# Kernel optimization log

Measured on AMD Instinct MI355X. Metric: run time of the kernel, lower is better.

## Reference

```python
import jax, jax.numpy as jnp
import numpy as np

N = 16384   # must equal C**2 so the rel-pos embed broadcasts with x
C = 128     # in_channels
K = 9       # k (min legal for C=128: (2k-1)^2 >= 2C-1)
C_OUT = 256


def setup_inputs() -> dict:
    key = jax.random.key(0)
    k1, k2, k3 = jax.random.split(key, 3)
    x = jax.random.normal(k1, (N, C), dtype=jnp.float32)
    rel_pos_table = jax.random.normal(k2, ((2 * K - 1) ** 2, C), dtype=jnp.float32) * 0.02
    W = jax.random.normal(k3, (2 * C, C_OUT), dtype=jnp.float32) / np.float32(np.sqrt(2 * C))
    b = jnp.zeros((C_OUT,), dtype=jnp.float32)
    return {"x": x, "rel_pos_table": rel_pos_table, "W": W, "b": b}


def _knn_indices(x, k):
    # brute-force kNN (torch_cluster knn_graph, loop=False), dilation=1 -> no edge subsampling
    sq = jnp.sum(x * x, axis=-1)                       # [N]
    d = sq[:, None] + sq[None, :] - 2.0 * (x @ x.T)    # [N, N] squared distances
    d = d.at[jnp.diag_indices(x.shape[0])].set(jnp.inf)  # exclude self-loops
    _, idx = jax.lax.top_k(-d, k)                      # [N, k] nearest neighbors
    return idx


def reference(x, rel_pos_table, W, b):
    n, c = x.shape
    # 1) graph built on RAW x (before rel-pos add), as in the torch forward
    nbr = _knn_indices(x, K)                           # [N, K]
    # 2) learnable relative positional embedding: grid_size = x.shape[1] = C
    ar = jnp.arange(c)
    rel = (ar[:, None] - ar[None, :] + c - 1).reshape(-1)  # [C*C] == [N]
    x = x + rel_pos_table[rel]                         # [N, C]
    # 3) MRConv: max-relative aggregation + concat + 1x1 linear
    x_j = x[nbr]                                       # [N, K, C] neighbor gather
    m = jnp.max(x_j - x[:, None, :], axis=1)           # [N, C] max over neighbors
    return jnp.concatenate([x, m], axis=-1) @ W + b    # [N, C_OUT]
```

## Files before the change

kernel.cpp:

```cpp
#include <hip/hip_runtime.h>

#define NPTS 16384
#define CH 128
#define KNN 9
#define NCAND 12
#define NHALF 4
#define COUT 256
#define RG 16
#define RCAND 3

typedef __attribute__((ext_vector_type(8))) short bf16x8;
typedef __attribute__((ext_vector_type(4))) float f32x4;
typedef __attribute__((address_space(1))) const unsigned gu32;
typedef __attribute__((address_space(3))) unsigned lu32;


__device__ __forceinline__ unsigned bfhi2(float x0, float x1) {
    unsigned u0 = __float_as_uint(x0), u1 = __float_as_uint(x1);
    unsigned r0 = (u0 + 0x7fffu + ((u0 >> 16) & 1u));
    unsigned r1 = (u1 + 0x7fffu + ((u1 >> 16) & 1u));
    return (r0 >> 16) | (r1 & 0xffff0000u);
}

struct TopL {
    float l0,l1,l2,l3,l4,l5,l6,l7,l8,l9,la,lb;
    int   m0,m1,m2,m3,m4,m5,m6,m7,m8,m9,ma,mb;
};
struct Top9 {
    float l0,l1,l2,l3,l4,l5,l6,l7,l8;
    int   m0,m1,m2,m3,m4,m5,m6,m7,m8;
};

__device__ __forceinline__ bool lexlt(float d, int g, float L, int M) {
    return d < L || (d == L && g < M);
}

__device__ __forceinline__ void ins12(TopL& T, float d, int g) {
    if (!lexlt(d, g, T.lb, T.mb)) return;
    bool b0 = lexlt(d,g,T.l0,T.m0);
    bool b1 = lexlt(d,g,T.l1,T.m1);
    bool b2 = lexlt(d,g,T.l2,T.m2);
    bool b3 = lexlt(d,g,T.l3,T.m3);
    bool b4 = lexlt(d,g,T.l4,T.m4);
    bool b5 = lexlt(d,g,T.l5,T.m5);
    bool b6 = lexlt(d,g,T.l6,T.m6);
    bool b7 = lexlt(d,g,T.l7,T.m7);
    bool b8 = lexlt(d,g,T.l8,T.m8);
    bool b9 = lexlt(d,g,T.l9,T.m9);
    bool ba = lexlt(d,g,T.la,T.ma);
    T.lb = ba ? T.la : d;               T.mb = ba ? T.ma : g;
    T.la = b9 ? T.l9 : (ba ? d : T.la); T.ma = b9 ? T.m9 : (ba ? g : T.ma);
    T.l9 = b8 ? T.l8 : (b9 ? d : T.l9); T.m9 = b8 ? T.m8 : (b9 ? g : T.m9);
    T.l8 = b7 ? T.l7 : (b8 ? d : T.l8); T.m8 = b7 ? T.m7 : (b8 ? g : T.m8);
    T.l7 = b6 ? T.l6 : (b7 ? d : T.l7); T.m7 = b6 ? T.m6 : (b7 ? g : T.m7);
    T.l6 = b5 ? T.l5 : (b6 ? d : T.l6); T.m6 = b5 ? T.m5 : (b6 ? g : T.m6);
    T.l5 = b4 ? T.l4 : (b5 ? d : T.l5); T.m5 = b4 ? T.m4 : (b5 ? g : T.m5);
    T.l4 = b3 ? T.l3 : (b4 ? d : T.l4); T.m4 = b3 ? T.m3 : (b4 ? g : T.m4);
    T.l3 = b2 ? T.l2 : (b3 ? d : T.l3); T.m3 = b2 ? T.m2 : (b3 ? g : T.m3);
    T.l2 = b1 ? T.l1 : (b2 ? d : T.l2); T.m2 = b1 ? T.m1 : (b2 ? g : T.m2);
    T.l1 = b0 ? T.l0 : (b1 ? d : T.l1); T.m1 = b0 ? T.m0 : (b1 ? g : T.m1);
    T.l0 = b0 ? d : T.l0;               T.m0 = b0 ? g : T.m0;
}

__device__ __forceinline__ void ins9(Top9& T, float d, int g) {
    if (!lexlt(d, g, T.l8, T.m8)) return;
    bool b0 = lexlt(d,g,T.l0,T.m0);
    bool b1 = lexlt(d,g,T.l1,T.m1);
    bool b2 = lexlt(d,g,T.l2,T.m2);
    bool b3 = lexlt(d,g,T.l3,T.m3);
    bool b4 = lexlt(d,g,T.l4,T.m4);
    bool b5 = lexlt(d,g,T.l5,T.m5);
    bool b6 = lexlt(d,g,T.l6,T.m6);
    bool b7 = lexlt(d,g,T.l7,T.m7);
    T.l8 = b7 ? T.l7 : d;               T.m8 = b7 ? T.m7 : g;
    T.l7 = b6 ? T.l6 : (b7 ? d : T.l7); T.m7 = b6 ? T.m6 : (b7 ? g : T.m7);
    T.l6 = b5 ? T.l5 : (b6 ? d : T.l6); T.m6 = b5 ? T.m5 : (b6 ? g : T.m6);
    T.l5 = b4 ? T.l4 : (b5 ? d : T.l5); T.m5 = b4 ? T.m4 : (b5 ? g : T.m5);
    T.l4 = b3 ? T.l3 : (b4 ? d : T.l4); T.m4 = b3 ? T.m3 : (b4 ? g : T.m4);
    T.l3 = b2 ? T.l2 : (b3 ? d : T.l3); T.m3 = b2 ? T.m2 : (b3 ? g : T.m3);
    T.l2 = b1 ? T.l1 : (b2 ? d : T.l2); T.m2 = b1 ? T.m1 : (b2 ? g : T.m2);
    T.l1 = b0 ? T.l0 : (b1 ? d : T.l1); T.m1 = b0 ? T.m0 : (b1 ? g : T.m1);
    T.l0 = b0 ? d : T.l0;               T.m0 = b0 ? g : T.m0;
}

__device__ __forceinline__ void merge_shfl(TopL& T, int mask) {
    TopL o;
    o.l0=__shfl_xor(T.l0,mask); o.m0=__shfl_xor(T.m0,mask);
    o.l1=__shfl_xor(T.l1,mask); o.m1=__shfl_xor(T.m1,mask);
    o.l2=__shfl_xor(T.l2,mask); o.m2=__shfl_xor(T.m2,mask);
    o.l3=__shfl_xor(T.l3,mask); o.m3=__shfl_xor(T.m3,mask);
    o.l4=__shfl_xor(T.l4,mask); o.m4=__shfl_xor(T.m4,mask);
    o.l5=__shfl_xor(T.l5,mask); o.m5=__shfl_xor(T.m5,mask);
    o.l6=__shfl_xor(T.l6,mask); o.m6=__shfl_xor(T.m6,mask);
    o.l7=__shfl_xor(T.l7,mask); o.m7=__shfl_xor(T.m7,mask);
    o.l8=__shfl_xor(T.l8,mask); o.m8=__shfl_xor(T.m8,mask);
    o.l9=__shfl_xor(T.l9,mask); o.m9=__shfl_xor(T.m9,mask);
    o.la=__shfl_xor(T.la,mask); o.ma=__shfl_xor(T.ma,mask);
    o.lb=__shfl_xor(T.lb,mask); o.mb=__shfl_xor(T.mb,mask);
    ins12(T,o.l0,o.m0); ins12(T,o.l1,o.m1); ins12(T,o.l2,o.m2);
    ins12(T,o.l3,o.m3); ins12(T,o.l4,o.m4); ins12(T,o.l5,o.m5);
    ins12(T,o.l6,o.m6); ins12(T,o.l7,o.m7); ins12(T,o.l8,o.m8);
    ins12(T,o.l9,o.m9); ins12(T,o.la,o.ma); ins12(T,o.lb,o.mb);
}

__device__ __forceinline__ void merge_shfl9(Top9& T, int mask) {
    Top9 o;
    o.l0=__shfl_xor(T.l0,mask); o.m0=__shfl_xor(T.m0,mask);
    o.l1=__shfl_xor(T.l1,mask); o.m1=__shfl_xor(T.m1,mask);
    o.l2=__shfl_xor(T.l2,mask); o.m2=__shfl_xor(T.m2,mask);
    o.l3=__shfl_xor(T.l3,mask); o.m3=__shfl_xor(T.m3,mask);
    o.l4=__shfl_xor(T.l4,mask); o.m4=__shfl_xor(T.m4,mask);
    o.l5=__shfl_xor(T.l5,mask); o.m5=__shfl_xor(T.m5,mask);
    o.l6=__shfl_xor(T.l6,mask); o.m6=__shfl_xor(T.m6,mask);
    o.l7=__shfl_xor(T.l7,mask); o.m7=__shfl_xor(T.m7,mask);
    o.l8=__shfl_xor(T.l8,mask); o.m8=__shfl_xor(T.m8,mask);
    ins9(T,o.l0,o.m0); ins9(T,o.l1,o.m1); ins9(T,o.l2,o.m2);
    ins9(T,o.l3,o.m3); ins9(T,o.l4,o.m4); ins9(T,o.l5,o.m5);
    ins9(T,o.l6,o.m6); ins9(T,o.l7,o.m7); ins9(T,o.l8,o.m8);
}

__global__ __launch_bounds__(256) void sqnp_kernel(const float* __restrict__ x,
                                                   float* __restrict__ sq) {
    const int i = blockIdx.x * 256 + threadIdx.x;
    const float4* row4 = (const float4*)(x + (size_t)i * CH);
    float r[8];
    {
        float4 a = row4[0], b = row4[1];
        r[0] = __fmul_rn(a.x, a.x); r[1] = __fmul_rn(a.y, a.y);
        r[2] = __fmul_rn(a.z, a.z); r[3] = __fmul_rn(a.w, a.w);
        r[4] = __fmul_rn(b.x, b.x); r[5] = __fmul_rn(b.y, b.y);
        r[6] = __fmul_rn(b.z, b.z); r[7] = __fmul_rn(b.w, b.w);
    }
#pragma unroll
    for (int g = 1; g < 16; ++g) {
        float4 a = row4[2 * g], b = row4[2 * g + 1];
        r[0] = __fadd_rn(r[0], __fmul_rn(a.x, a.x));
        r[1] = __fadd_rn(r[1], __fmul_rn(a.y, a.y));
        r[2] = __fadd_rn(r[2], __fmul_rn(a.z, a.z));
        r[3] = __fadd_rn(r[3], __fmul_rn(a.w, a.w));
        r[4] = __fadd_rn(r[4], __fmul_rn(b.x, b.x));
        r[5] = __fadd_rn(r[5], __fmul_rn(b.y, b.y));
        r[6] = __fadd_rn(r[6], __fmul_rn(b.z, b.z));
        r[7] = __fadd_rn(r[7], __fmul_rn(b.w, b.w));
    }
    float t0 = __fadd_rn(__fadd_rn(r[0], r[1]), __fadd_rn(r[2], r[3]));
    float t1 = __fadd_rn(__fadd_rn(r[4], r[5]), __fadd_rn(r[6], r[7]));
    sq[i] = __fadd_rn(t0, t1);
}

__global__ __launch_bounds__(256) void split_kernel(const float* __restrict__ x,
                                                    short* __restrict__ xhi) {
    const int P = blockIdx.x * 256 + threadIdx.x;
    const int r = P >> 4;
    const int s = P & 15;
    const int phys = s ^ (r & 15);
    const float4* src = (const float4*)(x + (size_t)r * CH) + s * 2;
    float4 f0 = src[0], f1 = src[1];
    uint4 h;
    h.x = bfhi2(f0.x, f0.y);
    h.y = bfhi2(f0.z, f0.w);
    h.z = bfhi2(f1.x, f1.y);
    h.w = bfhi2(f1.z, f1.w);
    *(uint4*)&xhi[(size_t)r * 128 + phys * 8] = h;
}

__global__ __launch_bounds__(256, 3) void knn_kernel(const short* __restrict__ xhi,
                                                     const float* __restrict__ sq,
                                                     unsigned short* __restrict__ cand) {
    __shared__ short Bhi[64 * 128];
    __shared__ float Dist[64 * 64];
    const int t = threadIdx.x;
    const int row0 = blockIdx.x * 64;
    const int half = blockIdx.y;
    const int ctbeg = half * (NPTS / NHALF);
    const int ctend = ctbeg + NPTS / NHALF;

    const int lane = t & 63;
    const int w = t >> 6;
    const int m = lane & 15;
    const int quad = lane >> 4;

#pragma unroll
    for (int it = 0; it < 4; ++it) {
        const int P = t + it * 256;
        __builtin_amdgcn_global_load_lds(
            (gu32*)&xhi[(size_t)ctbeg * 128 + P * 8],
            (lu32*)&Bhi[(it * 256 + w * 64) * 8], 16, 0, 0);
    }
    const short* arow = xhi + (size_t)(row0 + 16 * w + m) * 128;
    const bf16x8 a0 = *(const bf16x8*)&arow[((0 * 4 + quad) ^ m) * 8];
    const bf16x8 a1 = *(const bf16x8*)&arow[((1 * 4 + quad) ^ m) * 8];
    const bf16x8 a2 = *(const bf16x8*)&arow[((2 * 4 + quad) ^ m) * 8];
    const bf16x8 a3 = *(const bf16x8*)&arow[((3 * 4 + quad) ^ m) * 8];

    TopL T;
    T.l0=T.l1=T.l2=T.l3=T.l4=T.l5=T.l6=T.l7=T.l8=T.l9=T.la=T.lb = __builtin_inff();
    T.m0=T.m1=T.m2=T.m3=T.m4=T.m5=T.m6=T.m7=T.m8=T.m9=T.ma=T.mb = 0x7fffffff;

    const int srow = t >> 2;
    const int sq4 = t & 3;
    const int srowg = row0 + srow;
    const float* drow = &Dist[srow * 64];
    const int sxor = srow & 63;

    float qd0 = __builtin_inff(), qd1 = __builtin_inff();
    int   qg0 = 0x7fffffff,      qg1 = 0x7fffffff;
    int   qn = 0;

    for (int ct = ctbeg; ct < ctend; ct += 64) {
        __syncthreads();

        const float sqc0 = sq[ct + 0  + m];
        const float sqc1 = sq[ct + 16 + m];
        const float sqc2 = sq[ct + 32 + m];
        const float sqc3 = sq[ct + 48 + m];

        f32x4 acc0 = {0.f,0.f,0.f,0.f};
        f32x4 acc1 = {0.f,0.f,0.f,0.f};
        f32x4 acc2 = {0.f,0.f,0.f,0.f};
        f32x4 acc3 = {0.f,0.f,0.f,0.f};

#pragma unroll
        for (int kc = 0; kc < 4; ++kc) {
            const int ks = ((kc * 4 + quad) ^ m) * 8;
            const bf16x8 ah = (kc == 0) ? a0 : (kc == 1) ? a1 : (kc == 2) ? a2 : a3;
            bf16x8 bh0 = *(const bf16x8*)&Bhi[(0  + m) * 128 + ks];
            bf16x8 bh1 = *(const bf16x8*)&Bhi[(16 + m) * 128 + ks];
            bf16x8 bh2 = *(const bf16x8*)&Bhi[(32 + m) * 128 + ks];
            bf16x8 bh3 = *(const bf16x8*)&Bhi[(48 + m) * 128 + ks];
            acc0 = __builtin_amdgcn_mfma_f32_16x16x32_bf16(ah, bh0, acc0, 0, 0, 0);
            acc1 = __builtin_amdgcn_mfma_f32_16x16x32_bf16(ah, bh1, acc1, 0, 0, 0);
            acc2 = __builtin_amdgcn_mfma_f32_16x16x32_bf16(ah, bh2, acc2, 0, 0, 0);
            acc3 = __builtin_amdgcn_mfma_f32_16x16x32_bf16(ah, bh3, acc3, 0, 0, 0);
        }

#pragma unroll
        for (int reg = 0; reg < 4; ++reg) {
            const int row = 16 * w + quad * 4 + reg;
            const int c0 = 0  + m;
            const int c1 = 16 + m;
            const int c2 = 32 + m;
            const int c3 = 48 + m;
            Dist[row * 64 + (c0 ^ row)] = __builtin_fmaf(-2.f, acc0[reg], sqc0);
            Dist[row * 64 + (c1 ^ row)] = __builtin_fmaf(-2.f, acc1[reg], sqc1);
            Dist[row * 64 + (c2 ^ row)] = __builtin_fmaf(-2.f, acc2[reg], sqc2);
            Dist[row * 64 + (c3 ^ row)] = __builtin_fmaf(-2.f, acc3[reg], sqc3);
        }
        __syncthreads();

        const int ctn = ct + 64;
        if (ctn < ctend) {
#pragma unroll
            for (int it = 0; it < 4; ++it) {
                const int P = t + it * 256;
                __builtin_amdgcn_global_load_lds(
                    (gu32*)&xhi[(size_t)ctn * 128 + P * 8],
                    (lu32*)&Bhi[(it * 256 + w * 64) * 8], 16, 0, 0);
            }
        }

#pragma unroll
        for (int k = 0; k < 16; ++k) {
            const int col = sq4 * 16 + k;
            const float d = drow[col ^ sxor];
            const int cg = ct + col;
            const bool pass = (d <= T.lb) && (cg != srowg);
            if (pass) {
                if (qn >= 2) {
                    ins12(T, d, cg);
                } else if (qn == 0) {
                    qd0 = d; qg0 = cg;
                } else {
                    qd1 = d; qg1 = cg;
                }
                ++qn;
            }
        }
        if (__any(qn >= 2)) {
            ins12(T, qd0, qg0);
            ins12(T, qd1, qg1);
            qd0 = qd1 = __builtin_inff();
            qg0 = qg1 = 0x7fffffff;
            qn = 0;
        }
    }

    ins12(T, qd0, qg0);
    ins12(T, qd1, qg1);
    merge_shfl(T, 1);
    merge_shfl(T, 2);

    if (sq4 == 0) {
        unsigned short* cp_out = cand + (size_t)srowg * (NHALF * NCAND) + half * NCAND;
        cp_out[0]=(unsigned short)T.m0; cp_out[1]=(unsigned short)T.m1;
        cp_out[2]=(unsigned short)T.m2; cp_out[3]=(unsigned short)T.m3;
        cp_out[4]=(unsigned short)T.m4; cp_out[5]=(unsigned short)T.m5;
        cp_out[6]=(unsigned short)T.m6; cp_out[7]=(unsigned short)T.m7;
        cp_out[8]=(unsigned short)T.m8; cp_out[9]=(unsigned short)T.m9;
        cp_out[10]=(unsigned short)T.ma; cp_out[11]=(unsigned short)T.mb;
    }
}

__global__ __launch_bounds__(256) void refine_np_kernel(const float* __restrict__ x,
                                                        const float* __restrict__ sq,
                                                        const unsigned short* __restrict__ cand,
                                                        unsigned short* __restrict__ nbr) {
    const int gt = blockIdx.x * 256 + threadIdx.x;
    const int i = gt >> 4;
    const int g = gt & (RG - 1);
    const float4* X4 = (const float4*)x;
    const float sqi = sq[i];

    int ci[RCAND];
#pragma unroll
    for (int m = 0; m < RCAND; ++m)
        ci[m] = (int)cand[i * (NHALF * NCAND) + g * RCAND + m];
    float dot[RCAND];
#pragma unroll
    for (int m = 0; m < RCAND; ++m) dot[m] = 0.f;
#pragma unroll 4
    for (int c4 = 0; c4 < 32; ++c4) {
        float4 xv = X4[(size_t)i * 32 + c4];
#pragma unroll
        for (int m = 0; m < RCAND; ++m) {
            float4 nv = X4[(size_t)ci[m] * 32 + c4];
            float a = dot[m];
            a = __builtin_fmaf(xv.x, nv.x, a);
            a = __builtin_fmaf(xv.y, nv.y, a);
            a = __builtin_fmaf(xv.z, nv.z, a);
            a = __builtin_fmaf(xv.w, nv.w, a);
            dot[m] = a;
        }
    }

    Top9 T;
    T.l0=T.l1=T.l2=T.l3=T.l4=T.l5=T.l6=T.l7=T.l8 = __builtin_inff();
    T.m0=T.m1=T.m2=T.m3=T.m4=T.m5=T.m6=T.m7=T.m8 = 0x7fffffff;
#pragma unroll
    for (int m = 0; m < RCAND; ++m) {
        float s = __fadd_rn(sqi, sq[ci[m]]);
        float d = __fsub_rn(s, __fmul_rn(2.0f, dot[m]));
        ins9(T, d, ci[m]);
    }

    merge_shfl9(T, 1);
    merge_shfl9(T, 2);
    merge_shfl9(T, 4);
    merge_shfl9(T, 8);

    if (g == 0) {
        unsigned short* np = nbr + (size_t)i * KNN;
        np[0]=(unsigned short)T.m0; np[1]=(unsigned short)T.m1; np[2]=(unsigned short)T.m2;
        np[3]=(unsigned short)T.m3; np[4]=(unsigned short)T.m4; np[5]=(unsigned short)T.m5;
        np[6]=(unsigned short)T.m6; np[7]=(unsigned short)T.m7; np[8]=(unsigned short)T.m8;
    }
}

__global__ __launch_bounds__(256, 2) void out_kernel(const float* __restrict__ x,
                                                     const float* __restrict__ tab,
                                                     const float* __restrict__ W,
                                                     const float* __restrict__ bias,
                                                     const unsigned short* __restrict__ nbr,
                                                     float* __restrict__ out) {
    __shared__ float cat[32][260];
    const int t = threadIdx.x;
    const int row0 = blockIdx.x * 32;
    {
        const int row = t >> 3;
        const int q = t & 7;
        const int i = row0 + row;
        const int rel_i = (i >> 7) - (i & 127) + 127;
        int nb[KNN], reln[KNN];
#pragma unroll
        for (int j = 0; j < KNN; ++j) {
            nb[j] = (int)nbr[i * KNN + j];
            reln[j] = (nb[j] >> 7) - (nb[j] & 127) + 127;
        }
        const float4* X4 = (const float4*)x;
        const float4* T4 = (const float4*)tab;
#pragma unroll
        for (int cc = 0; cc < 4; ++cc) {
            const int c4 = q * 4 + cc;
            float4 xv = X4[i * 32 + c4];
            float4 tv = T4[rel_i * 32 + c4];
            float4 xi;
            xi.x = xv.x + tv.x; xi.y = xv.y + tv.y; xi.z = xv.z + tv.z; xi.w = xv.w + tv.w;
            const float ninf = -__builtin_inff();
            float4 mx = {ninf, ninf, ninf, ninf};
#pragma unroll
            for (int j = 0; j < KNN; ++j) {
                float4 nv = X4[nb[j] * 32 + c4];
                float4 ntv = T4[reln[j] * 32 + c4];
                mx.x = fmaxf(mx.x, nv.x + ntv.x - xi.x);
                mx.y = fmaxf(mx.y, nv.y + ntv.y - xi.y);
                mx.z = fmaxf(mx.z, nv.z + ntv.z - xi.z);
                mx.w = fmaxf(mx.w, nv.w + ntv.w - xi.w);
            }
            *(float4*)&cat[row][c4 * 4] = xi;
            *(float4*)&cat[row][CH + c4 * 4] = mx;
        }
    }
    __syncthreads();

    float acc[32];
    const float bo = bias[t];
#pragma unroll
    for (int i = 0; i < 32; ++i) acc[i] = bo;
#pragma unroll 2
    for (int c0 = 0; c0 < 2 * CH; c0 += 4) {
        const float w0 = W[(c0 + 0) * COUT + t];
        const float w1 = W[(c0 + 1) * COUT + t];
        const float w2 = W[(c0 + 2) * COUT + t];
        const float w3 = W[(c0 + 3) * COUT + t];
#pragma unroll
        for (int i = 0; i < 32; ++i) {
            const float4 cv = *(const float4*)&cat[i][c0];
            acc[i] = fmaf(cv.x, w0, acc[i]);
            acc[i] = fmaf(cv.y, w1, acc[i]);
            acc[i] = fmaf(cv.z, w2, acc[i]);
            acc[i] = fmaf(cv.w, w3, acc[i]);
        }
    }
#pragma unroll
    for (int i = 0; i < 32; ++i) out[(size_t)(row0 + i) * COUT + t] = acc[i];
}

extern "C" void kernel_launch(void* const* d_in, const int* in_sizes, int n_in,
                              void* d_out, int out_size, void* d_ws, size_t ws_size,
                              hipStream_t stream) {
    (void)in_sizes; (void)n_in; (void)out_size; (void)ws_size;
    const float* x = (const float*)d_in[0];
    const float* tab = (const float*)d_in[1];
    const float* W = (const float*)d_in[2];
    const float* b = (const float*)d_in[3];
    float* out = (float*)d_out;

    char* ws = (char*)d_ws;
    float* sq = (float*)ws;
    unsigned short* nbr = (unsigned short*)(sq + NPTS);

    short* xhi = (short*)d_out;
    unsigned short* cand = (unsigned short*)((char*)d_out + ((size_t)NPTS * CH * 2));

    sqnp_kernel<<<NPTS / 256, 256, 0, stream>>>(x, sq);
    split_kernel<<<NPTS * 16 / 256, 256, 0, stream>>>(x, xhi);
    knn_kernel<<<dim3(NPTS / 64, NHALF), 256, 0, stream>>>(xhi, sq, cand);
    refine_np_kernel<<<NPTS * RG / 256, 256, 0, stream>>>(x, sq, cand, nbr);
    out_kernel<<<NPTS / 32, 256, 0, stream>>>(x, tab, W, b, nbr, out);
}
```

Baseline: 632.7 us.

## Select kNN candidates directly from MFMA registers and split candidate range eightfold

The kNN kernel no longer stages the distance tile through a shared-memory Dist buffer. The MFMA operands are swapped so each lane holds distances for its own query row, and each lane filters candidates straight from the accumulator registers, with top-12 lists merged across quads by shuffles. The candidate range is also split into 8 slices instead of 4, with refine candidates scaled to match, to add grid parallelism. This removes LDS writes, reads and bank traffic and frees LDS for occupancy, at the cost of more candidates to refine and larger per-row candidate output.

```diff
diff --git a/kernel.cpp b/kernel.cpp
--- a/kernel.cpp
+++ b/kernel.cpp
@@ -4,10 +4,10 @@
 #define CH 128
 #define KNN 9
 #define NCAND 12
-#define NHALF 4
+#define NHALF 8
 #define COUT 256
 #define RG 16
-#define RCAND 3
+#define RCAND 6
 
 typedef __attribute__((ext_vector_type(8))) short bf16x8;
 typedef __attribute__((ext_vector_type(4))) float f32x4;
@@ -168,7 +168,6 @@
                                                      const float* __restrict__ sq,
                                                      unsigned short* __restrict__ cand) {
     __shared__ short Bhi[64 * 128];
-    __shared__ float Dist[64 * 64];
     const int t = threadIdx.x;
     const int row0 = blockIdx.x * 64;
     const int half = blockIdx.y;
@@ -187,21 +186,17 @@
             (gu32*)&xhi[(size_t)ctbeg * 128 + P * 8],
             (lu32*)&Bhi[(it * 256 + w * 64) * 8], 16, 0, 0);
     }
-    const short* arow = xhi + (size_t)(row0 + 16 * w + m) * 128;
-    const bf16x8 a0 = *(const bf16x8*)&arow[((0 * 4 + quad) ^ m) * 8];
-    const bf16x8 a1 = *(const bf16x8*)&arow[((1 * 4 + quad) ^ m) * 8];
-    const bf16x8 a2 = *(const bf16x8*)&arow[((2 * 4 + quad) ^ m) * 8];
-    const bf16x8 a3 = *(const bf16x8*)&arow[((3 * 4 + quad) ^ m) * 8];
+    const short* qrow = xhi + (size_t)(row0 + 16 * w + m) * 128;
+    const bf16x8 a0 = *(const bf16x8*)&qrow[((0 * 4 + quad) ^ m) * 8];
+    const bf16x8 a1 = *(const bf16x8*)&qrow[((1 * 4 + quad) ^ m) * 8];
+    const bf16x8 a2 = *(const bf16x8*)&qrow[((2 * 4 + quad) ^ m) * 8];
+    const bf16x8 a3 = *(const bf16x8*)&qrow[((3 * 4 + quad) ^ m) * 8];
 
     TopL T;
     T.l0=T.l1=T.l2=T.l3=T.l4=T.l5=T.l6=T.l7=T.l8=T.l9=T.la=T.lb = __builtin_inff();
     T.m0=T.m1=T.m2=T.m3=T.m4=T.m5=T.m6=T.m7=T.m8=T.m9=T.ma=T.mb = 0x7fffffff;
 
-    const int srow = t >> 2;
-    const int sq4 = t & 3;
-    const int srowg = row0 + srow;
-    const float* drow = &Dist[srow * 64];
-    const int sxor = srow & 63;
+    const int qglob = row0 + 16 * w + m;
 
     float qd0 = __builtin_inff(), qd1 = __builtin_inff();
     int   qg0 = 0x7fffffff,      qg1 = 0x7fffffff;
@@ -209,11 +204,6 @@
 
     for (int ct = ctbeg; ct < ctend; ct += 64) {
         __syncthreads();
-
-        const float sqc0 = sq[ct + 0  + m];
-        const float sqc1 = sq[ct + 16 + m];
-        const float sqc2 = sq[ct + 32 + m];
-        const float sqc3 = sq[ct + 48 + m];
 
         f32x4 acc0 = {0.f,0.f,0.f,0.f};
         f32x4 acc1 = {0.f,0.f,0.f,0.f};
@@ -228,23 +218,10 @@
             bf16x8 bh1 = *(const bf16x8*)&Bhi[(16 + m) * 128 + ks];
             bf16x8 bh2 = *(const bf16x8*)&Bhi[(32 + m) * 128 + ks];
             bf16x8 bh3 = *(const bf16x8*)&Bhi[(48 + m) * 128 + ks];
-            acc0 = __builtin_amdgcn_mfma_f32_16x16x32_bf16(ah, bh0, acc0, 0, 0, 0);
-            acc1 = __builtin_amdgcn_mfma_f32_16x16x32_bf16(ah, bh1, acc1, 0, 0, 0);
-            acc2 = __builtin_amdgcn_mfma_f32_16x16x32_bf16(ah, bh2, acc2, 0, 0, 0);
-            acc3 = __builtin_amdgcn_mfma_f32_16x16x32_bf16(ah, bh3, acc3, 0, 0, 0);
-        }
-
-#pragma unroll
-        for (int reg = 0; reg < 4; ++reg) {
-            const int row = 16 * w + quad * 4 + reg;
-            const int c0 = 0  + m;
-            const int c1 = 16 + m;
-            const int c2 = 32 + m;
-            const int c3 = 48 + m;
-            Dist[row * 64 + (c0 ^ row)] = __builtin_fmaf(-2.f, acc0[reg], sqc0);
-            Dist[row * 64 + (c1 ^ row)] = __builtin_fmaf(-2.f, acc1[reg], sqc1);
-            Dist[row * 64 + (c2 ^ row)] = __builtin_fmaf(-2.f, acc2[reg], sqc2);
-            Dist[row * 64 + (c3 ^ row)] = __builtin_fmaf(-2.f, acc3[reg], sqc3);
+            acc0 = __builtin_amdgcn_mfma_f32_16x16x32_bf16(bh0, ah, acc0, 0, 0, 0);
+            acc1 = __builtin_amdgcn_mfma_f32_16x16x32_bf16(bh1, ah, acc1, 0, 0, 0);
+            acc2 = __builtin_amdgcn_mfma_f32_16x16x32_bf16(bh2, ah, acc2, 0, 0, 0);
+            acc3 = __builtin_amdgcn_mfma_f32_16x16x32_bf16(bh3, ah, acc3, 0, 0, 0);
         }
         __syncthreads();
 
@@ -260,20 +237,27 @@
         }
 
 #pragma unroll
-        for (int k = 0; k < 16; ++k) {
-            const int col = sq4 * 16 + k;
-            const float d = drow[col ^ sxor];
-            const int cg = ct + col;
-            const bool pass = (d <= T.lb) && (cg != srowg);
-            if (pass) {
-                if (qn >= 2) {
-                    ins12(T, d, cg);
-                } else if (qn == 0) {
-                    qd0 = d; qg0 = cg;
-                } else {
-                    qd1 = d; qg1 = cg;
+        for (int cg = 0; cg < 4; ++cg) {
+            const f32x4 ac = (cg == 0) ? acc0 : (cg == 1) ? acc1
+                           : (cg == 2) ? acc2 : acc3;
+            const float4 s4 = *(const float4*)&sq[ct + cg * 16 + quad * 4];
+#pragma unroll
+            for (int reg = 0; reg < 4; ++reg) {
+                const float sv = (reg == 0) ? s4.x : (reg == 1) ? s4.y
+                               : (reg == 2) ? s4.z : s4.w;
+                const float d = __builtin_fmaf(-2.f, ac[reg], sv);
+                const int cgi = ct + cg * 16 + quad * 4 + reg;
+                const bool pass = (d <= T.lb) && (cgi != qglob);
+                if (pass) {
+                    if (qn >= 2) {
+                        ins12(T, d, cgi);
+                    } else if (qn == 0) {
+                        qd0 = d; qg0 = cgi;
+                    } else {
+                        qd1 = d; qg1 = cgi;
+                    }
+                    ++qn;
                 }
-                ++qn;
             }
         }
         if (__any(qn >= 2)) {
@@ -287,11 +271,11 @@
 
     ins12(T, qd0, qg0);
     ins12(T, qd1, qg1);
-    merge_shfl(T, 1);
-    merge_shfl(T, 2);
-
-    if (sq4 == 0) {
-        unsigned short* cp_out = cand + (size_t)srowg * (NHALF * NCAND) + half * NCAND;
+    merge_shfl(T, 16);
+    merge_shfl(T, 32);
+
+    if (quad == 0) {
+        unsigned short* cp_out = cand + (size_t)qglob * (NHALF * NCAND) + half * NCAND;
         cp_out[0]=(unsigned short)T.m0; cp_out[1]=(unsigned short)T.m1;
         cp_out[2]=(unsigned short)T.m2; cp_out[3]=(unsigned short)T.m3;
         cp_out[4]=(unsigned short)T.m4; cp_out[5]=(unsigned short)T.m5;
```

Result: slower. 829.8 us (+31.2%).
